# Optimization experiments

Measured on AMD Instinct MI355X. Metric: run time of the kernel, lower is better.

Reference implementation:

```python
import jax, jax.numpy as jnp
import numpy as np

HOP = 128
NFFT = 256
SR = 16000
EPS = 1e-7
MIN_DB = -80.0


def _a_weighting_db():
    # librosa.fft_frequencies + librosa.A_weighting (min_db=-80), computed statically in numpy
    f = np.fft.rfftfreq(NFFT, d=1.0 / SR)  # [NFFT//2+1]
    c = np.array([12194.217, 20.598997, 107.65265, 737.86223]) ** 2.0
    f2 = f ** 2.0
    w = 2.0 + 20.0 * (
        np.log10(c[0])
        + 2.0 * np.log10(np.maximum(f2, 1e-30))
        - np.log10(f2 + c[0])
        - np.log10(f2 + c[1])
        - 0.5 * np.log10(f2 + c[2])
        - 0.5 * np.log10(f2 + c[3])
    )
    return np.maximum(w, MIN_DB).astype(np.float32)


def _loudness(x):
    # x: [B, C, T] -> channel mean -> librosa-style centered STFT (hann, reflect pad)
    x = jnp.mean(x, axis=1)  # [B, T]
    T = x.shape[1]
    pad = NFFT // 2
    xp = jnp.pad(x, ((0, 0), (pad, pad)), mode='reflect')  # [B, T+NFFT]
    n_frames = 1 + T // HOP
    idx = jnp.arange(n_frames)[:, None] * HOP + jnp.arange(NFFT)[None, :]  # [F, NFFT]
    frames = xp[:, idx]  # [B, F, NFFT]
    # periodic hann window (scipy fftbins=True, librosa default)
    win = (0.5 - 0.5 * jnp.cos(2.0 * jnp.pi * jnp.arange(NFFT) / NFFT)).astype(x.dtype)
    spec = jnp.fft.rfft(frames * win, axis=-1)  # [B, F, NFFT//2+1] complex
    log_mag = jnp.log(jnp.abs(spec) + EPS)  # [B, F, NFREQ]
    aw = jnp.asarray(_a_weighting_db())  # [NFREQ]
    # mean over frequency axis, then trailing singleton like original unsqueeze(-1)
    loud = jnp.mean(log_mag + aw[None, None, :], axis=-1)  # [B, F]
    return loud[..., None].astype(jnp.float32)


def setup_inputs() -> dict:
    key = jax.random.key(0)
    x = jax.random.normal(key, (64, 1, 640000), dtype=jnp.float32)
    return {"x": x}


def reference(x):
    return _loudness(x)
```

## Files before the change

### kernel.cpp

```cpp
#include <hip/hip_runtime.h>
#include <math.h>

#define HOP 128
#define T_LEN 640000
#define N_FRAMES 5001
#define N_PAIRS 2501
#define NB 64
#define GPB 16
#define MP 4
#define NBLK 2501

#define RE_SLOT 18
#define RE_GRP  164
#define IM_SLOT 18
#define IM_GRP  146

typedef float v2f __attribute__((ext_vector_type(2)));

static __device__ __forceinline__ v2f mk2(float a, float b) { v2f r; r.x = a; r.y = b; return r; }
static __device__ __forceinline__ v2f sp(float s) { v2f r; r.x = s; r.y = s; return r; }

static __device__ __forceinline__ float rsum16(float v) {
    v += __int_as_float(__builtin_amdgcn_update_dpp(0, __float_as_int(v), 0xB1, 0xF, 0xF, true));
    v += __int_as_float(__builtin_amdgcn_update_dpp(0, __float_as_int(v), 0x4E, 0xF, 0xF, true));
    v += __int_as_float(__builtin_amdgcn_update_dpp(0, __float_as_int(v), 0x141, 0xF, 0xF, true));
    v += __int_as_float(__builtin_amdgcn_update_dpp(0, __float_as_int(v), 0x140, 0xF, 0xF, true));
    return v;
}

__global__ __launch_bounds__(256) void loudness_kernel(const float* __restrict__ x,
                                                       float* __restrict__ out) {
    constexpr float C16[16] = {
        1.0f,  0.9238795325112867f,  0.7071067811865476f,  0.3826834323650898f,
        0.0f, -0.3826834323650898f, -0.7071067811865476f, -0.9238795325112867f,
       -1.0f, -0.9238795325112867f, -0.7071067811865476f, -0.3826834323650898f,
        0.0f,  0.3826834323650898f,  0.7071067811865476f,  0.9238795325112867f};
    constexpr float S16[16] = {
        0.0f,  0.3826834323650898f,  0.7071067811865476f,  0.9238795325112867f,
        1.0f,  0.9238795325112867f,  0.7071067811865476f,  0.3826834323650898f,
        0.0f, -0.3826834323650898f, -0.7071067811865476f, -0.9238795325112867f,
       -1.0f, -0.9238795325112867f, -0.7071067811865476f, -0.3826834323650898f};
    const float R2  = 0.7071067811865476f;
    const float c1v = 0.9238795325112867f, s1v = 0.3826834323650898f;
    const float c3v = 0.3826834323650898f, s3v = 0.9238795325112867f;
    const float CP8 = 0.9238795325112867f, SP8 = 0.3826834323650898f;
    const float K2  = 1.8477590650225735f;

    __shared__ alignas(16) v2f s_re[16 * RE_GRP];
    __shared__ alignas(16) v2f s_im[16 * IM_GRP];
    __shared__ v2f   s_stp[16];
    __shared__ float s_aw8[16];
    __shared__ float s_aw128;

    const int tid = threadIdx.x;

    {
        const float TP = 0.02454369260617026f;
        if (tid < 16) {
            float s, c;
            sincosf((float)tid * TP, &s, &c);
            s_stp[tid] = mk2(c, -s);
        }
        if (tid < 129) {
            const float LG2_10 = 0.30102999566398f;
            float fq = (float)tid * 62.5f;
            float f2 = fq * fq;
            const float a0 = 12194.217f * 12194.217f;
            const float a1 = 20.598997f * 20.598997f;
            const float a2 = 107.65265f * 107.65265f;
            const float a3 = 737.86223f * 737.86223f;
            float w = 2.0f + 20.0f * LG2_10 *
                      (__builtin_amdgcn_logf(a0) + 2.0f * __builtin_amdgcn_logf(fmaxf(f2, 1e-30f))
                     - __builtin_amdgcn_logf(f2 + a0) - __builtin_amdgcn_logf(f2 + a1)
                     - 0.5f * __builtin_amdgcn_logf(f2 + a2) - 0.5f * __builtin_amdgcn_logf(f2 + a3));
            ((float*)&s_im[0])[tid] = fmaxf(w, -80.0f);
        }
    }
    __syncthreads();
    if (tid < 16) {
        const float* scr = (const float*)&s_im[0];
        float s = 0.f;
#pragma unroll
        for (int k2 = 0; k2 < 8; ++k2) s += scr[tid + 16 * k2];
        s_aw8[tid] = s;
        if (tid == 0) s_aw128 = scr[128];
    }
    __syncthreads();
    s_im[(tid >> 4) * IM_GRP + (tid & 15)] = sp(0.f);
    __syncthreads();

    const int g = tid >> 4;
    const int r = tid & 15;

    const v2f   stp   = s_stp[r];
    const float aw8r  = s_aw8[r];
    const float aw128 = s_aw128;

    v2f twr[16];
    twr[0] = mk2(1.f, 0.f);
    twr[1] = stp;
#pragma unroll
    for (int w = 2; w < 16; ++w) {
        const v2f t = twr[w - 1];
        twr[w] = mk2(t.x * stp.x - t.y * stp.y, t.x * stp.y + t.y * stp.x);
    }

    float win16[16];
    {
        float cm2 = stp.x;
        float cm1 = stp.x * CP8 + stp.y * SP8;
        win16[0] = 0.5f - 0.5f * cm2;
        win16[1] = 0.5f - 0.5f * cm1;
#pragma unroll
        for (int n = 2; n < 16; ++n) {
            const float c = K2 * cm1 - cm2;
            win16[n] = 0.5f - 0.5f * c;
            cm2 = cm1; cm1 = c;
        }
    }

    const int rp  = (r <= 8) ? r : 16 - r;
    const int rp7 = rp & 7;
    const v2f sgnv = sp((r <= 8) ? 1.f : -1.f);
    v2f* __restrict__ reW = &s_re[g * RE_GRP + r];
    v2f* __restrict__ imW = &s_im[g * IM_GRP + r];
    const float4* __restrict__ reCol = (const float4*)&s_re[g * RE_GRP + RE_SLOT * rp];
    const float4* __restrict__ imCol = (const float4*)&s_im[g * IM_GRP + IM_SLOT * rp7];

    const int p0 = (blockIdx.x * GPB + g) * MP;
    const float HALF_LN2 = 0.34657359027997264f;

#pragma unroll 1
    for (int it = 0; it < MP; ++it) {
        const int p  = p0 + it;
        const int b  = p / N_PAIRS;
        const int pp = p - b * N_PAIRS;
        const int fA = 2 * pp;
        const int fB = (fA < 5000) ? fA + 1 : 5000;
        const int dB = (fB - fA) * HOP;
        const float* __restrict__ xb = x + (size_t)b * T_LEN;

        v2f xw[16];
        const int base = fA * HOP - HOP + r;
        if (pp >= 1 && pp <= 2499) {
            const float* __restrict__ xp = xb + base;
#pragma unroll
            for (int n2 = 0; n2 < 16; ++n2) {
                const int o = 16 * n2;
                xw[n2] = mk2(xp[o], xp[o + dB]) * sp(win16[n2]);
            }
        } else {
#pragma unroll
            for (int n2 = 0; n2 < 16; ++n2) {
                int jA = base + 16 * n2;
                int jB = jA + dB;
                jA = (jA < 0) ? -jA : jA;
                jA = (jA >= T_LEN) ? (2 * T_LEN - 2 - jA) : jA;
                jB = (jB < 0) ? -jB : jB;
                jB = (jB >= T_LEN) ? (2 * T_LEN - 2 - jB) : jB;
                xw[n2] = mk2(xb[jA], xb[jB]) * sp(win16[n2]);
            }
        }

        v2f pv[8], qv[8];
#pragma unroll
        for (int n = 1; n <= 7; ++n) { pv[n] = xw[n] + xw[16 - n]; qv[n] = xw[n] - xw[16 - n]; }
        const v2f bse = xw[0] + xw[8];
        const v2f d08 = xw[0] - xw[8];
        const v2f se  = pv[2] + pv[4] + pv[6];
        const v2f so  = pv[1] + pv[3] + pv[5] + pv[7];
        const v2f r0  = bse + se + so;
        const v2f r8  = bse + se - so;
        v2f rre[8], rim[8];
#pragma unroll
        for (int k1 = 1; k1 <= 7; ++k1) {
            v2f re = (k1 & 1) ? d08 : bse;
            v2f im = sp(0.f);
#pragma unroll
            for (int n = 1; n <= 7; ++n) {
                const int m = (k1 * n) & 15;
                re += pv[n] * sp(C16[m]);
                im -= qv[n] * sp(S16[m]);
            }
            rre[k1] = re;
            rim[k1] = im;
        }

        reW[0] = r0;
#pragma unroll
        for (int k = 1; k <= 7; ++k) {
            reW[RE_SLOT * k] = rre[k];
            imW[IM_SLOT * k] = rim[k];
        }
        reW[RE_SLOT * 8] = r8;

        v2f bbx[16], bby[16];
#pragma unroll
        for (int j = 0; j < 8; ++j) {
            const float4 R4v = reCol[j];
            const float4 I4v = imCol[j];
            {
                const int w = 2 * j;
                const v2f xx = mk2(R4v.x, R4v.y);
                const v2f yy = mk2(I4v.x, I4v.y) * sgnv;
                if (j == 0) { bbx[0] = xx; bby[0] = yy; }
                else {
                    bbx[w] = xx * sp(twr[w].x) - yy * sp(twr[w].y);
                    bby[w] = xx * sp(twr[w].y) + yy * sp(twr[w].x);
                }
            }
            {
                const int w = 2 * j + 1;
                const v2f xx = mk2(R4v.z, R4v.w);
                const v2f yy = mk2(I4v.z, I4v.w) * sgnv;
                bbx[w] = xx * sp(twr[w].x) - yy * sp(twr[w].y);
                bby[w] = xx * sp(twr[w].y) + yy * sp(twr[w].x);
            }
        }

#pragma unroll
        for (int j = 0; j < 8; ++j) {
            const v2f ux = bbx[j], uy = bby[j], vx = bbx[j + 8], vy = bby[j + 8];
            bbx[j] = ux + vx; bby[j] = uy + vy;
            const v2f dx = ux - vx, dy = uy - vy;
            v2f ox, oy;
            if      (j == 0) { ox = dx;                              oy = dy; }
            else if (j == 1) { ox =  dx * sp(c1v) + dy * sp(s1v);    oy =  dy * sp(c1v) - dx * sp(s1v); }
            else if (j == 2) { ox = (dx + dy) * sp(R2);              oy = (dy - dx) * sp(R2); }
            else if (j == 3) { ox =  dx * sp(c3v) + dy * sp(s3v);    oy =  dy * sp(c3v) - dx * sp(s3v); }
            else if (j == 4) { ox = dy;                              oy = sp(0.f) - dx; }
            else if (j == 5) { ox = dy * sp(s3v) - dx * sp(c3v);     oy = sp(0.f) - dy * sp(c3v) - dx * sp(s3v); }
            else if (j == 6) { ox = (dy - dx) * sp(R2);              oy = sp(0.f) - (dx + dy) * sp(R2); }
            else             { ox = dy * sp(s1v) - dx * sp(c1v);     oy = sp(0.f) - dy * sp(c1v) - dx * sp(s1v); }
            bbx[j + 8] = ox; bby[j + 8] = oy;
        }
#pragma unroll
        for (int h = 0; h <= 8; h += 8) {
#pragma unroll
            for (int j = 0; j < 4; ++j) {
                const v2f ux = bbx[h + j], uy = bby[h + j], vx = bbx[h + j + 4], vy = bby[h + j + 4];
                bbx[h + j] = ux + vx; bby[h + j] = uy + vy;
                const v2f dx = ux - vx, dy = uy - vy;
                v2f ox, oy;
                if      (j == 0) { ox = dx;                  oy = dy; }
                else if (j == 1) { ox = (dx + dy) * sp(R2);  oy = (dy - dx) * sp(R2); }
                else if (j == 2) { ox = dy;                  oy = sp(0.f) - dx; }
                else             { ox = (dy - dx) * sp(R2);  oy = sp(0.f) - (dx + dy) * sp(R2); }
                bbx[h + j + 4] = ox; bby[h + j + 4] = oy;
            }
        }
#pragma unroll
        for (int gg = 0; gg < 16; gg += 4) {
            {
                const v2f ux = bbx[gg], uy = bby[gg], vx = bbx[gg + 2], vy = bby[gg + 2];
                bbx[gg] = ux + vx;     bby[gg] = uy + vy;
                bbx[gg + 2] = ux - vx; bby[gg + 2] = uy - vy;
            }
            {
                const v2f ux = bbx[gg + 1], uy = bby[gg + 1], vx = bbx[gg + 3], vy = bby[gg + 3];
                bbx[gg + 1] = ux + vx; bby[gg + 1] = uy + vy;
                const v2f dx = ux - vx, dy = uy - vy;
                bbx[gg + 3] = dy; bby[gg + 3] = sp(0.f) - dx;
            }
        }

        v2f m2[8];
#pragma unroll
        for (int t = 0; t < 8; ++t) {
            const v2f Yx = bbx[2 * t] + bbx[2 * t + 1];
            const v2f Yy = bby[2 * t] + bby[2 * t + 1];
            m2[t] = Yx * Yx + Yy * Yy + sp(1e-14f);
        }
        const v2f P0 = m2[0] * m2[1], P1 = m2[2] * m2[3], P2 = m2[4] * m2[5], P3 = m2[6] * m2[7];
        const float lA = __builtin_amdgcn_logf(P0.x) + __builtin_amdgcn_logf(P1.x)
                       + __builtin_amdgcn_logf(P2.x) + __builtin_amdgcn_logf(P3.x);
        const float lB = __builtin_amdgcn_logf(P0.y) + __builtin_amdgcn_logf(P1.y)
                       + __builtin_amdgcn_logf(P2.y) + __builtin_amdgcn_logf(P3.y);
        v2f ssum = sp(HALF_LN2) * mk2(lA, lB) + sp(aw8r);

        const v2f d0 = bbx[0] - bbx[1];
        if (r == 0) {
            ssum += sp(HALF_LN2) * mk2(__builtin_amdgcn_logf(d0.x * d0.x + 1e-14f),
                                       __builtin_amdgcn_logf(d0.y * d0.y + 1e-14f))
                  + sp(aw128);
        }

        ssum.x = rsum16(ssum.x);
        ssum.y = rsum16(ssum.y);

        if (r == 0) {
            out[b * N_FRAMES + fA] = ssum.x * (1.0f / 129.0f);
            out[b * N_FRAMES + fB] = ssum.y * (1.0f / 129.0f);
        }
    }
}

extern "C" void kernel_launch(void* const* d_in, const int* in_sizes, int n_in,
                              void* d_out, int out_size, void* d_ws, size_t ws_size,
                              hipStream_t stream) {
    const float* x = (const float*)d_in[0];
    float* out = (float*)d_out;
    loudness_kernel<<<NBLK, 256, 0, stream>>>(x, out);
}
```

Measured before the change: 61.22 us.

## Move twiddle and A-weight setup to separate kernel, one pair per group

A one-block setup kernel now computes the twiddle table and A-weight partial sums into workspace, so each main block no longer runs sincos/log or its per-block barriers. The main kernel drops the 4-pairs-per-group loop and launches four times as many blocks, each group handling a single frame pair. The imaginary scratch buffer is shrunk, and a sign factor replaces the old zero-initialised slots. The cost is an extra kernel launch, less work per block to amortise the remaining setup, and a dependency on the workspace buffer.

```diff
diff --git a/kernel.cpp b/kernel.cpp
--- a/kernel.cpp
+++ b/kernel.cpp
@@ -7,13 +7,11 @@
 #define N_PAIRS 2501
 #define NB 64
 #define GPB 16
-#define MP 4
-#define NBLK 2501
 
 #define RE_SLOT 18
 #define RE_GRP  164
 #define IM_SLOT 18
-#define IM_GRP  146
+#define IM_GRP  132
 
 typedef float v2f __attribute__((ext_vector_type(2)));
 
@@ -28,8 +26,43 @@
     return v;
 }
 
+__global__ __launch_bounds__(256) void setup_kernel(float* __restrict__ ws) {
+    __shared__ float s_aw[132];
+    const int tid = threadIdx.x;
+    const float TP = 0.02454369260617026f;
+    {
+        const int w = tid >> 4, rr = tid & 15;
+        float s, c;
+        sincosf((float)(rr * w) * TP, &s, &c);
+        ((v2f*)ws)[tid] = mk2(c, -s);
+    }
+    if (tid < 129) {
+        const float LG2_10 = 0.30102999566398f;
+        float fq = (float)tid * 62.5f;
+        float f2 = fq * fq;
+        const float a0 = 12194.217f * 12194.217f;
+        const float a1 = 20.598997f * 20.598997f;
+        const float a2 = 107.65265f * 107.65265f;
+        const float a3 = 737.86223f * 737.86223f;
+        float w = 2.0f + 20.0f * LG2_10 *
+                  (__builtin_amdgcn_logf(a0) + 2.0f * __builtin_amdgcn_logf(fmaxf(f2, 1e-30f))
+                 - __builtin_amdgcn_logf(f2 + a0) - __builtin_amdgcn_logf(f2 + a1)
+                 - 0.5f * __builtin_amdgcn_logf(f2 + a2) - 0.5f * __builtin_amdgcn_logf(f2 + a3));
+        s_aw[tid] = fmaxf(w, -80.0f);
+    }
+    __syncthreads();
+    if (tid < 16) {
+        float s = 0.f;
+#pragma unroll
+        for (int k2 = 0; k2 < 8; ++k2) s += s_aw[tid + 16 * k2];
+        ws[512 + tid] = s;
+        if (tid == 0) ws[528] = s_aw[128];
+    }
+}
+
 __global__ __launch_bounds__(256) void loudness_kernel(const float* __restrict__ x,
-                                                       float* __restrict__ out) {
+                                                       float* __restrict__ out,
+                                                       const float* __restrict__ ws) {
     constexpr float C16[16] = {
         1.0f,  0.9238795325112867f,  0.7071067811865476f,  0.3826834323650898f,
         0.0f, -0.3826834323650898f, -0.7071067811865476f, -0.9238795325112867f,
@@ -48,62 +81,16 @@
 
     __shared__ alignas(16) v2f s_re[16 * RE_GRP];
     __shared__ alignas(16) v2f s_im[16 * IM_GRP];
-    __shared__ v2f   s_stp[16];
-    __shared__ float s_aw8[16];
-    __shared__ float s_aw128;
+    __shared__ v2f s_twT[256];
 
     const int tid = threadIdx.x;
-
-    {
-        const float TP = 0.02454369260617026f;
-        if (tid < 16) {
-            float s, c;
-            sincosf((float)tid * TP, &s, &c);
-            s_stp[tid] = mk2(c, -s);
-        }
-        if (tid < 129) {
-            const float LG2_10 = 0.30102999566398f;
-            float fq = (float)tid * 62.5f;
-            float f2 = fq * fq;
-            const float a0 = 12194.217f * 12194.217f;
-            const float a1 = 20.598997f * 20.598997f;
-            const float a2 = 107.65265f * 107.65265f;
-            const float a3 = 737.86223f * 737.86223f;
-            float w = 2.0f + 20.0f * LG2_10 *
-                      (__builtin_amdgcn_logf(a0) + 2.0f * __builtin_amdgcn_logf(fmaxf(f2, 1e-30f))
-                     - __builtin_amdgcn_logf(f2 + a0) - __builtin_amdgcn_logf(f2 + a1)
-                     - 0.5f * __builtin_amdgcn_logf(f2 + a2) - 0.5f * __builtin_amdgcn_logf(f2 + a3));
-            ((float*)&s_im[0])[tid] = fmaxf(w, -80.0f);
-        }
-    }
-    __syncthreads();
-    if (tid < 16) {
-        const float* scr = (const float*)&s_im[0];
-        float s = 0.f;
-#pragma unroll
-        for (int k2 = 0; k2 < 8; ++k2) s += scr[tid + 16 * k2];
-        s_aw8[tid] = s;
-        if (tid == 0) s_aw128 = scr[128];
-    }
-    __syncthreads();
-    s_im[(tid >> 4) * IM_GRP + (tid & 15)] = sp(0.f);
-    __syncthreads();
-
     const int g = tid >> 4;
     const int r = tid & 15;
 
-    const v2f   stp   = s_stp[r];
-    const float aw8r  = s_aw8[r];
-    const float aw128 = s_aw128;
-
-    v2f twr[16];
-    twr[0] = mk2(1.f, 0.f);
-    twr[1] = stp;
-#pragma unroll
-    for (int w = 2; w < 16; ++w) {
-        const v2f t = twr[w - 1];
-        twr[w] = mk2(t.x * stp.x - t.y * stp.y, t.x * stp.y + t.y * stp.x);
-    }
+    s_twT[tid] = ((const v2f*)ws)[tid];
+    const float aw8r  = ws[512 + r];
+    const float aw128 = ws[528];
+    const v2f stp = ((const v2f*)ws)[16 + r];
 
     float win16[16];
     {
@@ -118,180 +105,178 @@
             cm2 = cm1; cm1 = c;
         }
     }
-
-    const int rp  = (r <= 8) ? r : 16 - r;
-    const int rp7 = rp & 7;
-    const v2f sgnv = sp((r <= 8) ? 1.f : -1.f);
-    v2f* __restrict__ reW = &s_re[g * RE_GRP + r];
-    v2f* __restrict__ imW = &s_im[g * IM_GRP + r];
-    const float4* __restrict__ reCol = (const float4*)&s_re[g * RE_GRP + RE_SLOT * rp];
-    const float4* __restrict__ imCol = (const float4*)&s_im[g * IM_GRP + IM_SLOT * rp7];
-
-    const int p0 = (blockIdx.x * GPB + g) * MP;
-    const float HALF_LN2 = 0.34657359027997264f;
-
-#pragma unroll 1
-    for (int it = 0; it < MP; ++it) {
-        const int p  = p0 + it;
-        const int b  = p / N_PAIRS;
-        const int pp = p - b * N_PAIRS;
-        const int fA = 2 * pp;
-        const int fB = (fA < 5000) ? fA + 1 : 5000;
-        const int dB = (fB - fA) * HOP;
-        const float* __restrict__ xb = x + (size_t)b * T_LEN;
-
-        v2f xw[16];
-        const int base = fA * HOP - HOP + r;
-        if (pp >= 1 && pp <= 2499) {
-            const float* __restrict__ xp = xb + base;
-#pragma unroll
-            for (int n2 = 0; n2 < 16; ++n2) {
-                const int o = 16 * n2;
-                xw[n2] = mk2(xp[o], xp[o + dB]) * sp(win16[n2]);
-            }
-        } else {
-#pragma unroll
-            for (int n2 = 0; n2 < 16; ++n2) {
-                int jA = base + 16 * n2;
-                int jB = jA + dB;
-                jA = (jA < 0) ? -jA : jA;
-                jA = (jA >= T_LEN) ? (2 * T_LEN - 2 - jA) : jA;
-                jB = (jB < 0) ? -jB : jB;
-                jB = (jB >= T_LEN) ? (2 * T_LEN - 2 - jB) : jB;
-                xw[n2] = mk2(xb[jA], xb[jB]) * sp(win16[n2]);
-            }
-        }
-
-        v2f pv[8], qv[8];
-#pragma unroll
-        for (int n = 1; n <= 7; ++n) { pv[n] = xw[n] + xw[16 - n]; qv[n] = xw[n] - xw[16 - n]; }
-        const v2f bse = xw[0] + xw[8];
-        const v2f d08 = xw[0] - xw[8];
-        const v2f se  = pv[2] + pv[4] + pv[6];
-        const v2f so  = pv[1] + pv[3] + pv[5] + pv[7];
-        const v2f r0  = bse + se + so;
-        const v2f r8  = bse + se - so;
-        v2f rre[8], rim[8];
-#pragma unroll
-        for (int k1 = 1; k1 <= 7; ++k1) {
-            v2f re = (k1 & 1) ? d08 : bse;
-            v2f im = sp(0.f);
-#pragma unroll
-            for (int n = 1; n <= 7; ++n) {
-                const int m = (k1 * n) & 15;
-                re += pv[n] * sp(C16[m]);
-                im -= qv[n] * sp(S16[m]);
-            }
-            rre[k1] = re;
-            rim[k1] = im;
-        }
-
+    __syncthreads();
+
+    const int gp = blockIdx.x * GPB + g;
+    const int b  = gp / N_PAIRS;
+    const int pp = gp - b * N_PAIRS;
+    const int fA = 2 * pp;
+    const int fB = (fA < 5000) ? fA + 1 : 5000;
+    const int dB = (fB - fA) * HOP;
+    const float* __restrict__ xb = x + (size_t)b * T_LEN;
+
+    v2f xw[16];
+    const int base = fA * HOP - HOP + r;
+    if (pp >= 1 && pp <= 2499) {
+        const float* __restrict__ xp = xb + base;
+#pragma unroll
+        for (int n2 = 0; n2 < 16; ++n2) {
+            const int o = 16 * n2;
+            xw[n2] = mk2(xp[o], xp[o + dB]) * sp(win16[n2]);
+        }
+    } else {
+#pragma unroll
+        for (int n2 = 0; n2 < 16; ++n2) {
+            int jA = base + 16 * n2;
+            int jB = jA + dB;
+            jA = (jA < 0) ? -jA : jA;
+            jA = (jA >= T_LEN) ? (2 * T_LEN - 2 - jA) : jA;
+            jB = (jB < 0) ? -jB : jB;
+            jB = (jB >= T_LEN) ? (2 * T_LEN - 2 - jB) : jB;
+            xw[n2] = mk2(xb[jA], xb[jB]) * sp(win16[n2]);
+        }
+    }
+
+    v2f pv[8], qv[8];
+#pragma unroll
+    for (int n = 1; n <= 7; ++n) { pv[n] = xw[n] + xw[16 - n]; qv[n] = xw[n] - xw[16 - n]; }
+    const v2f bse = xw[0] + xw[8];
+    const v2f d08 = xw[0] - xw[8];
+    const v2f se  = pv[2] + pv[4] + pv[6];
+    const v2f so  = pv[1] + pv[3] + pv[5] + pv[7];
+    const v2f r0  = bse + se + so;
+    const v2f r8  = bse + se - so;
+    v2f rre[8], rim[8];
+#pragma unroll
+    for (int k1 = 1; k1 <= 7; ++k1) {
+        v2f re = (k1 & 1) ? d08 : bse;
+        v2f im = sp(0.f);
+#pragma unroll
+        for (int n = 1; n <= 7; ++n) {
+            const int m = (k1 * n) & 15;
+            re += pv[n] * sp(C16[m]);
+            im -= qv[n] * sp(S16[m]);
+        }
+        rre[k1] = re;
+        rim[k1] = im;
+    }
+
+    {
+        v2f* __restrict__ reW = &s_re[g * RE_GRP + r];
+        v2f* __restrict__ imW = &s_im[g * IM_GRP + r];
         reW[0] = r0;
 #pragma unroll
         for (int k = 1; k <= 7; ++k) {
             reW[RE_SLOT * k] = rre[k];
-            imW[IM_SLOT * k] = rim[k];
+            imW[IM_SLOT * (k - 1)] = rim[k];
         }
         reW[RE_SLOT * 8] = r8;
-
-        v2f bbx[16], bby[16];
-#pragma unroll
-        for (int j = 0; j < 8; ++j) {
-            const float4 R4v = reCol[j];
-            const float4 I4v = imCol[j];
-            {
-                const int w = 2 * j;
-                const v2f xx = mk2(R4v.x, R4v.y);
-                const v2f yy = mk2(I4v.x, I4v.y) * sgnv;
-                if (j == 0) { bbx[0] = xx; bby[0] = yy; }
-                else {
-                    bbx[w] = xx * sp(twr[w].x) - yy * sp(twr[w].y);
-                    bby[w] = xx * sp(twr[w].y) + yy * sp(twr[w].x);
-                }
-            }
-            {
-                const int w = 2 * j + 1;
-                const v2f xx = mk2(R4v.z, R4v.w);
-                const v2f yy = mk2(I4v.z, I4v.w) * sgnv;
-                bbx[w] = xx * sp(twr[w].x) - yy * sp(twr[w].y);
-                bby[w] = xx * sp(twr[w].y) + yy * sp(twr[w].x);
-            }
-        }
-
-#pragma unroll
-        for (int j = 0; j < 8; ++j) {
-            const v2f ux = bbx[j], uy = bby[j], vx = bbx[j + 8], vy = bby[j + 8];
-            bbx[j] = ux + vx; bby[j] = uy + vy;
+    }
+
+    const int rp  = (r <= 8) ? r : 16 - r;
+    const int rpi = (rp >= 1 && rp <= 7) ? (rp - 1) : 0;
+    const float ysgn = (r == 0 || r == 8) ? 0.f : ((r < 8) ? 1.f : -1.f);
+    const float4* __restrict__ reCol = (const float4*)&s_re[g * RE_GRP + RE_SLOT * rp];
+    const float4* __restrict__ imCol = (const float4*)&s_im[g * IM_GRP + IM_SLOT * rpi];
+    const v2f* __restrict__ twp = &s_twT[r];
+
+    v2f bbx[16], bby[16];
+#pragma unroll
+    for (int j = 0; j < 8; ++j) {
+        const float4 R4v = reCol[j];
+        const float4 I4v = imCol[j];
+        {
+            const int w = 2 * j;
+            const v2f tw = twp[16 * w];
+            const v2f xx = mk2(R4v.x, R4v.y);
+            const v2f yy = mk2(I4v.x, I4v.y) * sp(ysgn);
+            bbx[w] = xx * sp(tw.x) - yy * sp(tw.y);
+            bby[w] = xx * sp(tw.y) + yy * sp(tw.x);
+        }
+        {
+            const int w = 2 * j + 1;
+            const v2f tw = twp[16 * w];
+            const v2f xx = mk2(R4v.z, R4v.w);
+            const v2f yy = mk2(I4v.z, I4v.w) * sp(ysgn);
+            bbx[w] = xx * sp(tw.x) - yy * sp(tw.y);
+            bby[w] = xx * sp(tw.y) + yy * sp(tw.x);
+        }
+    }
+
+#pragma unroll
+    for (int j = 0; j < 8; ++j) {
+        const v2f ux = bbx[j], uy = bby[j], vx = bbx[j + 8], vy = bby[j + 8];
+        bbx[j] = ux + vx; bby[j] = uy + vy;
+        const v2f dx = ux - vx, dy = uy - vy;
+        v2f ox, oy;
+        if      (j == 0) { ox = dx;                              oy = dy; }
+        else if (j == 1) { ox =  dx * sp(c1v) + dy * sp(s1v);    oy =  dy * sp(c1v) - dx * sp(s1v); }
+        else if (j == 2) { ox = (dx + dy) * sp(R2);              oy = (dy - dx) * sp(R2); }
+        else if (j == 3) { ox =  dx * sp(c3v) + dy * sp(s3v);    oy =  dy * sp(c3v) - dx * sp(s3v); }
+        else if (j == 4) { ox = dy;                              oy = sp(0.f) - dx; }
+        else if (j == 5) { ox = dy * sp(s3v) - dx * sp(c3v);     oy = sp(0.f) - dy * sp(c3v) - dx * sp(s3v); }
+        else if (j == 6) { ox = (dy - dx) * sp(R2);              oy = sp(0.f) - (dx + dy) * sp(R2); }
+        else             { ox = dy * sp(s1v) - dx * sp(c1v);     oy = sp(0.f) - dy * sp(c1v) - dx * sp(s1v); }
+        bbx[j + 8] = ox; bby[j + 8] = oy;
+    }
+#pragma unroll
+    for (int h = 0; h <= 8; h += 8) {
+#pragma unroll
+        for (int j = 0; j < 4; ++j) {
+            const v2f ux = bbx[h + j], uy = bby[h + j], vx = bbx[h + j + 4], vy = bby[h + j + 4];
+            bbx[h + j] = ux + vx; bby[h + j] = uy + vy;
             const v2f dx = ux - vx, dy = uy - vy;
             v2f ox, oy;
-            if      (j == 0) { ox = dx;                              oy = dy; }
-            else if (j == 1) { ox =  dx * sp(c1v) + dy * sp(s1v);    oy =  dy * sp(c1v) - dx * sp(s1v); }
-            else if (j == 2) { ox = (dx + dy) * sp(R2);              oy = (dy - dx) * sp(R2); }
-            else if (j == 3) { ox =  dx * sp(c3v) + dy * sp(s3v);    oy =  dy * sp(c3v) - dx * sp(s3v); }
-            else if (j == 4) { ox = dy;                              oy = sp(0.f) - dx; }
-            else if (j == 5) { ox = dy * sp(s3v) - dx * sp(c3v);     oy = sp(0.f) - dy * sp(c3v) - dx * sp(s3v); }
-            else if (j == 6) { ox = (dy - dx) * sp(R2);              oy = sp(0.f) - (dx + dy) * sp(R2); }
-            else             { ox = dy * sp(s1v) - dx * sp(c1v);     oy = sp(0.f) - dy * sp(c1v) - dx * sp(s1v); }
-            bbx[j + 8] = ox; bby[j + 8] = oy;
-        }
-#pragma unroll
-        for (int h = 0; h <= 8; h += 8) {
-#pragma unroll
-            for (int j = 0; j < 4; ++j) {
-                const v2f ux = bbx[h + j], uy = bby[h + j], vx = bbx[h + j + 4], vy = bby[h + j + 4];
-                bbx[h + j] = ux + vx; bby[h + j] = uy + vy;
-                const v2f dx = ux - vx, dy = uy - vy;
-                v2f ox, oy;
-                if      (j == 0) { ox = dx;                  oy = dy; }
-                else if (j == 1) { ox = (dx + dy) * sp(R2);  oy = (dy - dx) * sp(R2); }
-                else if (j == 2) { ox = dy;                  oy = sp(0.f) - dx; }
-                else             { ox = (dy - dx) * sp(R2);  oy = sp(0.f) - (dx + dy) * sp(R2); }
-                bbx[h + j + 4] = ox; bby[h + j + 4] = oy;
-            }
-        }
-#pragma unroll
-        for (int gg = 0; gg < 16; gg += 4) {
-            {
-                const v2f ux = bbx[gg], uy = bby[gg], vx = bbx[gg + 2], vy = bby[gg + 2];
-                bbx[gg] = ux + vx;     bby[gg] = uy + vy;
-                bbx[gg + 2] = ux - vx; bby[gg + 2] = uy - vy;
-            }
-            {
-                const v2f ux = bbx[gg + 1], uy = bby[gg + 1], vx = bbx[gg + 3], vy = bby[gg + 3];
-                bbx[gg + 1] = ux + vx; bby[gg + 1] = uy + vy;
-                const v2f dx = ux - vx, dy = uy - vy;
-                bbx[gg + 3] = dy; bby[gg + 3] = sp(0.f) - dx;
-            }
-        }
-
-        v2f m2[8];
-#pragma unroll
-        for (int t = 0; t < 8; ++t) {
-            const v2f Yx = bbx[2 * t] + bbx[2 * t + 1];
-            const v2f Yy = bby[2 * t] + bby[2 * t + 1];
-            m2[t] = Yx * Yx + Yy * Yy + sp(1e-14f);
-        }
-        const v2f P0 = m2[0] * m2[1], P1 = m2[2] * m2[3], P2 = m2[4] * m2[5], P3 = m2[6] * m2[7];
-        const float lA = __builtin_amdgcn_logf(P0.x) + __builtin_amdgcn_logf(P1.x)
-                       + __builtin_amdgcn_logf(P2.x) + __builtin_amdgcn_logf(P3.x);
-        const float lB = __builtin_amdgcn_logf(P0.y) + __builtin_amdgcn_logf(P1.y)
-                       + __builtin_amdgcn_logf(P2.y) + __builtin_amdgcn_logf(P3.y);
-        v2f ssum = sp(HALF_LN2) * mk2(lA, lB) + sp(aw8r);
-
-        const v2f d0 = bbx[0] - bbx[1];
-        if (r == 0) {
-            ssum += sp(HALF_LN2) * mk2(__builtin_amdgcn_logf(d0.x * d0.x + 1e-14f),
-                                       __builtin_amdgcn_logf(d0.y * d0.y + 1e-14f))
-                  + sp(aw128);
-        }
-
-        ssum.x = rsum16(ssum.x);
-        ssum.y = rsum16(ssum.y);
-
-        if (r == 0) {
-            out[b * N_FRAMES + fA] = ssum.x * (1.0f / 129.0f);
-            out[b * N_FRAMES + fB] = ssum.y * (1.0f / 129.0f);
-        }
+            if      (j == 0) { ox = dx;                  oy = dy; }
+            else if (j == 1) { ox = (dx + dy) * sp(R2);  oy = (dy - dx) * sp(R2); }
+            else if (j == 2) { ox = dy;                  oy = sp(0.f) - dx; }
+            else             { ox = (dy - dx) * sp(R2);  oy = sp(0.f) - (dx + dy) * sp(R2); }
+            bbx[h + j + 4] = ox; bby[h + j + 4] = oy;
+        }
+    }
+#pragma unroll
+    for (int gg = 0; gg < 16; gg += 4) {
+        {
+            const v2f ux = bbx[gg], uy = bby[gg], vx = bbx[gg + 2], vy = bby[gg + 2];
+            bbx[gg] = ux + vx;     bby[gg] = uy + vy;
+            bbx[gg + 2] = ux - vx; bby[gg + 2] = uy - vy;
+        }
+        {
+            const v2f ux = bbx[gg + 1], uy = bby[gg + 1], vx = bbx[gg + 3], vy = bby[gg + 3];
+            bbx[gg + 1] = ux + vx; bby[gg + 1] = uy + vy;
+            const v2f dx = ux - vx, dy = uy - vy;
+            bbx[gg + 3] = dy; bby[gg + 3] = sp(0.f) - dx;
+        }
+    }
+
+    const float HALF_LN2 = 0.34657359027997264f;
+    v2f m2[8];
+#pragma unroll
+    for (int t = 0; t < 8; ++t) {
+        const v2f Yx = bbx[2 * t] + bbx[2 * t + 1];
+        const v2f Yy = bby[2 * t] + bby[2 * t + 1];
+        m2[t] = Yx * Yx + Yy * Yy + sp(1e-14f);
+    }
+    const v2f P0 = m2[0] * m2[1], P1 = m2[2] * m2[3], P2 = m2[4] * m2[5], P3 = m2[6] * m2[7];
+    const float lA = __builtin_amdgcn_logf(P0.x) + __builtin_amdgcn_logf(P1.x)
+                   + __builtin_amdgcn_logf(P2.x) + __builtin_amdgcn_logf(P3.x);
+    const float lB = __builtin_amdgcn_logf(P0.y) + __builtin_amdgcn_logf(P1.y)
+                   + __builtin_amdgcn_logf(P2.y) + __builtin_amdgcn_logf(P3.y);
+    v2f ssum = sp(HALF_LN2) * mk2(lA, lB) + sp(aw8r);
+
+    const v2f d0 = bbx[0] - bbx[1];
+    if (r == 0) {
+        ssum += sp(HALF_LN2) * mk2(__builtin_amdgcn_logf(d0.x * d0.x + 1e-14f),
+                                   __builtin_amdgcn_logf(d0.y * d0.y + 1e-14f))
+              + sp(aw128);
+    }
+
+    ssum.x = rsum16(ssum.x);
+    ssum.y = rsum16(ssum.y);
+
+    if (r == 0) {
+        out[b * N_FRAMES + fA] = ssum.x * (1.0f / 129.0f);
+        out[b * N_FRAMES + fB] = ssum.y * (1.0f / 129.0f);
     }
 }
 
@@ -300,5 +285,7 @@
                               hipStream_t stream) {
     const float* x = (const float*)d_in[0];
     float* out = (float*)d_out;
-    loudness_kernel<<<NBLK, 256, 0, stream>>>(x, out);
-}
+    float* ws = (float*)d_ws;
+    setup_kernel<<<1, 256, 0, stream>>>(ws);
+    loudness_kernel<<<(NB * N_PAIRS) / GPB, 256, 0, stream>>>(x, out, ws);
+}
```

After: 55.48 us. 1.1x faster.
